# Performance work log

Hardware: AMD Instinct MI355X
Metric: run time of the kernel (lower is better)

Reference implementation:

```python
import jax, jax.numpy as jnp
import numpy as np

N = 50000   # nodes
E = 600000  # edges
D = 128     # in_neurons
H = 128     # hidden_neurons
O = 64      # output_neurons
G = 512     # graphs in batch
BN_EPS = 1e-5


def _linear_params(key, fan_in, fan_out):
    kw, kb = jax.random.split(key)
    s = 1.0 / np.sqrt(fan_in)
    W = jax.random.uniform(kw, (fan_out, fan_in), jnp.float32, -s, s)
    b = jax.random.uniform(kb, (fan_out,), jnp.float32, -s, s)
    return W, b


def setup_inputs() -> dict:
    key = jax.random.key(0)
    ks = jax.random.split(key, 12)
    inp = {}
    inp["x"] = jax.random.normal(ks[0], (N, D), jnp.float32)
    inp["edge_index"] = jax.random.randint(ks[1], (2, E), 0, N, jnp.int64)
    inp["batch"] = jnp.sort(jax.random.randint(ks[2], (N,), 0, G, jnp.int64))
    # GIN layer 1 (D->H->H), BN1
    inp["W11"], inp["b11"] = _linear_params(ks[3], D, H)
    inp["W12"], inp["b12"] = _linear_params(ks[4], H, H)
    inp["g1"], inp["be1"] = jnp.ones((H,), jnp.float32), jnp.zeros((H,), jnp.float32)
    # GIN layer 2
    inp["W21"], inp["b21"] = _linear_params(ks[5], H, H)
    inp["W22"], inp["b22"] = _linear_params(ks[6], H, H)
    inp["g2"], inp["be2"] = jnp.ones((H,), jnp.float32), jnp.zeros((H,), jnp.float32)
    # GIN layer 3
    inp["W31"], inp["b31"] = _linear_params(ks[7], H, H)
    inp["W32"], inp["b32"] = _linear_params(ks[8], H, H)
    inp["g3"], inp["be3"] = jnp.ones((H,), jnp.float32), jnp.zeros((H,), jnp.float32)
    # final projection (3H -> O)
    inp["linW"], inp["linb"] = _linear_params(ks[9], 3 * H, O)
    return inp


def reference(x, edge_index, batch,
              W11, b11, W12, b12, g1, be1,
              W21, b21, W22, b22, g2, be2,
              W31, b31, W32, b32, g3, be3,
              linW, linb):
    src, dst = edge_index[0], edge_index[1]

    def gin_conv(h, Wa, ba, Wb, bb):
        # GIN (eps=0): mlp((1+eps)*h + sum_{j in N(i)} h_j)
        agg = jax.ops.segment_sum(h[src], dst, num_segments=N)
        z = h + agg
        z = jax.nn.relu(z @ Wa.T + ba)
        return z @ Wb.T + bb

    def batch_norm(h, g, b):
        # training-mode BatchNorm1d: per-feature batch stats (biased var)
        mu = jnp.mean(h, axis=0)
        var = jnp.var(h, axis=0)
        return g * (h - mu) * jax.lax.rsqrt(var + BN_EPS) + b

    h1 = jax.nn.relu(batch_norm(gin_conv(x, W11, b11, W12, b12), g1, be1))
    h2 = jax.nn.relu(batch_norm(gin_conv(h1, W21, b21, W22, b22), g2, be2))
    h3 = jax.nn.relu(batch_norm(gin_conv(h2, W31, b31, W32, b32), g3, be3))

    counts = jax.ops.segment_sum(jnp.ones((N,), jnp.float32), batch, num_segments=G)
    counts = jnp.maximum(counts, 1.0)[:, None]  # [G, 1]

    def mean_pool(h):
        return jax.ops.segment_sum(h, batch, num_segments=G) / counts

    h_final = jnp.concatenate([mean_pool(h1), mean_pool(h2), mean_pool(h3)], axis=1)  # [G, 3H]
    out = h_final @ linW.T + linb  # [G, O]
    # F.normalize(dim=1): divide by L2 norm clamped to eps=1e-12
    nrm = jnp.maximum(jnp.linalg.norm(out, axis=1, keepdims=True), 1e-12)
    return out / nrm
```

## Files before the change

### kernel.cpp

```cpp
#include <hip/hip_runtime.h>

#define NN 50000
#define NE 600000
#define HD 128
#define NG 512
#define OD 64
#define BN_EPS 1e-5f

#define SCAN_BLK 1024
#define NSB ((NN + SCAN_BLK - 1) / SCAN_BLK)
#define ECAP 1536
#define NBANK 8

typedef __attribute__((ext_vector_type(8))) short bf16x8;
typedef __attribute__((ext_vector_type(4))) float f32x4;

__device__ __forceinline__ unsigned short f2bf(float f) {
    unsigned u = __builtin_bit_cast(unsigned, f);
    unsigned r = u + 0x7FFFu + ((u >> 16) & 1u);
    return (unsigned short)(r >> 16);
}

__device__ __forceinline__ float bflo(unsigned u) { return __builtin_bit_cast(float, u << 16); }
__device__ __forceinline__ float bfhi(unsigned u) { return __builtin_bit_cast(float, u & 0xffff0000u); }

__device__ __forceinline__ unsigned packbf2(float x, float y) {
    return (unsigned)f2bf(x) | ((unsigned)f2bf(y) << 16);
}


__global__ void cvt_kernel(const float* __restrict__ src, unsigned short* __restrict__ dst, int n8) {
    int i = blockIdx.x * blockDim.x + threadIdx.x;
    if (i >= n8) return;
    float4 a = ((const float4*)src)[2 * i];
    float4 b = ((const float4*)src)[2 * i + 1];
    uint4 o;
    o.x = packbf2(a.x, a.y);
    o.y = packbf2(a.z, a.w);
    o.z = packbf2(b.x, b.y);
    o.w = packbf2(b.z, b.w);
    ((uint4*)dst)[i] = o;
}

__global__ void cvt6_kernel(const float* __restrict__ s0, const float* __restrict__ s1,
                            const float* __restrict__ s2, const float* __restrict__ s3,
                            const float* __restrict__ s4, const float* __restrict__ s5,
                            unsigned short* __restrict__ dst) {
    int i = blockIdx.x * blockDim.x + threadIdx.x;
    const int wsel = i >> 11;
    const int o8 = i & 2047;
    const float* sp = (wsel == 0) ? s0 : (wsel == 1) ? s1 : (wsel == 2) ? s2
                    : (wsel == 3) ? s3 : (wsel == 4) ? s4 : s5;
    float4 a = ((const float4*)sp)[2 * o8];
    float4 b = ((const float4*)sp)[2 * o8 + 1];
    uint4 o;
    o.x = packbf2(a.x, a.y);
    o.y = packbf2(a.z, a.w);
    o.z = packbf2(b.x, b.y);
    o.w = packbf2(b.z, b.w);
    ((uint4*)(dst + (size_t)wsel * HD * HD))[o8] = o;
}


__global__ void hist_kernel(const int* __restrict__ dst, int* __restrict__ deg, int E) {
    int i = blockIdx.x * blockDim.x + threadIdx.x;
    if (i < E) atomicAdd(&deg[dst[i]], 1);
}

__global__ void local_scan_kernel(const int* __restrict__ deg, int* __restrict__ lexcl,
                                  int* __restrict__ bsum, int n) {
    __shared__ int part[SCAN_BLK];
    const int tid = threadIdx.x;
    const int i = blockIdx.x * SCAN_BLK + tid;
    int v = (i < n) ? deg[i] : 0;
    part[tid] = v;
    __syncthreads();
    int incl = v;
    for (int off = 1; off < SCAN_BLK; off <<= 1) {
        int t = (tid >= off) ? part[tid - off] : 0;
        __syncthreads();
        incl += t;
        part[tid] = incl;
        __syncthreads();
    }
    if (i < n) lexcl[i] = incl - v;
    if (tid == SCAN_BLK - 1) bsum[blockIdx.x] = incl;
}

__global__ void scan_bsum_kernel(const int* __restrict__ bsum, int* __restrict__ boff,
                                 int* __restrict__ offsets, int nb, int n) {
    const int tid = threadIdx.x;
    int orig = (tid < nb) ? bsum[tid] : 0;
    int v = orig;
    for (int off = 1; off < 64; off <<= 1) {
        int t = __shfl_up(v, off);
        if (tid >= off) v += t;
    }
    if (tid < nb) boff[tid] = v - orig;
    if (tid == 63) offsets[n] = v;
}

__global__ void finalize_gstart_kernel(const int* __restrict__ lexcl, const int* __restrict__ boff,
                                       int* __restrict__ offsets, int* __restrict__ cursor,
                                       const int* __restrict__ batch, int* __restrict__ gstart,
                                       int n, int G) {
    int i = blockIdx.x * blockDim.x + threadIdx.x;
    if (i >= n) return;
    int o = lexcl[i] + boff[i >> 10];
    offsets[i] = o;
    cursor[i] = o;
    int b = batch[i];
    int bp = (i == 0) ? -1 : batch[i - 1];
    for (int g = bp + 1; g <= b; ++g) gstart[g] = i;
    if (i == n - 1) {
        for (int g = b + 1; g <= G; ++g) gstart[g] = n;
    }
}

__global__ void fill_kernel(const int* __restrict__ src, const int* __restrict__ dst,
                            int* __restrict__ cursor, int* __restrict__ srcs, int E) {
    int i = blockIdx.x * blockDim.x + threadIdx.x;
    if (i < E) {
        int pos = atomicAdd(&cursor[dst[i]], 1);
        srcs[pos] = src[i];
    }
}


__global__ __launch_bounds__(512) void fused_gin(const unsigned* __restrict__ hp,
                                                 const int* __restrict__ offsets,
                                                 const int* __restrict__ srcs,
                                                 const unsigned short* __restrict__ WaBf,
                                                 const float* __restrict__ ba,
                                                 const unsigned short* __restrict__ WbBf,
                                                 const float* __restrict__ bb,
                                                 unsigned short* __restrict__ Cb,
                                                 float* __restrict__ statsOut,
                                                 int nrows) {
    __shared__ short SB[64 * 136];
    __shared__ int elds[ECAP];
    __shared__ float sred[2][128][2];

    const int t = threadIdx.x;
    const int lane = t & 63;
    const int w = t >> 6;
    const int g16 = lane >> 4;
    const int c16 = lane & 15;
    const int row0 = blockIdx.x * 64;

    const int rend = (row0 + 64 < nrows) ? row0 + 64 : nrows;
    const int ebase = offsets[row0];
    const int cnt = offsets[rend] - ebase;
    const bool fast = (cnt <= ECAP);

    if (fast) {
        for (int k = t; k < cnt; k += 512) elds[k] = srcs[ebase + k];
    }
    __syncthreads();

    for (int i = 0; i < 8; ++i) {
        const int r = w * 8 + i;
        const int grow = row0 + r;
        float a0 = 0.f, a1 = 0.f, a2 = 0.f, a3 = 0.f;
        float a4 = 0.f, a5 = 0.f, a6 = 0.f, a7 = 0.f;

        auto acc8 = [&](uint4 v) {
            a0 += bflo(v.x); a1 += bfhi(v.x);
            a2 += bflo(v.y); a3 += bfhi(v.y);
            a4 += bflo(v.z); a5 += bfhi(v.z);
            a6 += bflo(v.w); a7 += bfhi(v.w);
        };
        auto ld4 = [&](int idx) -> uint4 {
            return ((const uint4*)(hp + (size_t)idx * 64))[c16];
        };

        if (grow < nrows) {
            const int jb = offsets[grow];
            const int items = offsets[grow + 1] - jb + 1;
            if (fast) {
                const int j0 = jb - ebase;
                uint4 v0 = {0, 0, 0, 0}, v1 = {0, 0, 0, 0}, v2 = {0, 0, 0, 0}, v3 = {0, 0, 0, 0};
                {
                    const int it = g16;
                    if (it < items) v0 = ld4(it == 0 ? grow : elds[j0 + it - 1]);
                }
                {
                    const int it = 4 + g16;
                    if (it < items) v1 = ld4(elds[j0 + it - 1]);
                }
                {
                    const int it = 8 + g16;
                    if (it < items) v2 = ld4(elds[j0 + it - 1]);
                }
                {
                    const int it = 12 + g16;
                    if (it < items) v3 = ld4(elds[j0 + it - 1]);
                }
                acc8(v0); acc8(v1); acc8(v2); acc8(v3);
                for (int base = 16; base < items; base += 4) {
                    const int it = base + g16;
                    uint4 v = {0, 0, 0, 0};
                    if (it < items) v = ld4(elds[j0 + it - 1]);
                    acc8(v);
                }
            } else {
                for (int base = 0; base < items; base += 4) {
                    const int it = base + g16;
                    uint4 v = {0, 0, 0, 0};
                    if (it < items) v = ld4(it == 0 ? grow : srcs[jb + it - 1]);
                    acc8(v);
                }
            }
        }
        a0 += __shfl_xor(a0, 16); a1 += __shfl_xor(a1, 16);
        a2 += __shfl_xor(a2, 16); a3 += __shfl_xor(a3, 16);
        a4 += __shfl_xor(a4, 16); a5 += __shfl_xor(a5, 16);
        a6 += __shfl_xor(a6, 16); a7 += __shfl_xor(a7, 16);
        a0 += __shfl_xor(a0, 32); a1 += __shfl_xor(a1, 32);
        a2 += __shfl_xor(a2, 32); a3 += __shfl_xor(a3, 32);
        a4 += __shfl_xor(a4, 32); a5 += __shfl_xor(a5, 32);
        a6 += __shfl_xor(a6, 32); a7 += __shfl_xor(a7, 32);
        if (g16 == 0) {
            uint4 o;
            o.x = packbf2(a0, a1);
            o.y = packbf2(a2, a3);
            o.z = packbf2(a4, a5);
            o.w = packbf2(a6, a7);
            *(uint4*)&SB[r * 136 + c16 * 8] = o;
        }
    }
    __syncthreads();

    const int wr = w >> 2;
    const int wc = w & 3;
    const int l15 = lane & 15;
    const int l4 = lane >> 4;

    f32x4 acc[2][2];
#pragma unroll
    for (int m = 0; m < 2; ++m)
#pragma unroll
        for (int n = 0; n < 2; ++n) acc[m][n] = (f32x4){0.f, 0.f, 0.f, 0.f};

#pragma unroll
    for (int kk = 0; kk < 4; ++kk) {
        bf16x8 af[2], bfr[2];
#pragma unroll
        for (int m = 0; m < 2; ++m)
            af[m] = *(const bf16x8*)&SB[(wr * 32 + m * 16 + l15) * 136 + kk * 32 + l4 * 8];
#pragma unroll
        for (int n = 0; n < 2; ++n)
            bfr[n] = *(const bf16x8*)(WaBf + (size_t)(wc * 32 + n * 16 + l15) * HD + kk * 32 + l4 * 8);
#pragma unroll
        for (int m = 0; m < 2; ++m)
#pragma unroll
            for (int n = 0; n < 2; ++n)
                acc[m][n] = __builtin_amdgcn_mfma_f32_16x16x32_bf16(af[m], bfr[n], acc[m][n], 0, 0, 0);
    }
    __syncthreads();

#pragma unroll
    for (int n = 0; n < 2; ++n) {
        const int col = wc * 32 + n * 16 + l15;
        const float bav = ba[col];
#pragma unroll
        for (int m = 0; m < 2; ++m) {
#pragma unroll
            for (int j = 0; j < 4; ++j) {
                const int row = wr * 32 + m * 16 + l4 * 4 + j;
                SB[row * 136 + col] = (short)f2bf(fmaxf(acc[m][n][j] + bav, 0.f));
            }
        }
    }
    __syncthreads();

#pragma unroll
    for (int m = 0; m < 2; ++m)
#pragma unroll
        for (int n = 0; n < 2; ++n) acc[m][n] = (f32x4){0.f, 0.f, 0.f, 0.f};

#pragma unroll
    for (int kk = 0; kk < 4; ++kk) {
        bf16x8 af[2], bfr[2];
#pragma unroll
        for (int m = 0; m < 2; ++m)
            af[m] = *(const bf16x8*)&SB[(wr * 32 + m * 16 + l15) * 136 + kk * 32 + l4 * 8];
#pragma unroll
        for (int n = 0; n < 2; ++n)
            bfr[n] = *(const bf16x8*)(WbBf + (size_t)(wc * 32 + n * 16 + l15) * HD + kk * 32 + l4 * 8);
#pragma unroll
        for (int m = 0; m < 2; ++m)
#pragma unroll
            for (int n = 0; n < 2; ++n)
                acc[m][n] = __builtin_amdgcn_mfma_f32_16x16x32_bf16(af[m], bfr[n], acc[m][n], 0, 0, 0);
    }

    float st00 = 0.f, st01 = 0.f, st10 = 0.f, st11 = 0.f;
#pragma unroll
    for (int n = 0; n < 2; ++n) {
        const int col = wc * 32 + n * 16 + l15;
        const float bbv = bb[col];
#pragma unroll
        for (int m = 0; m < 2; ++m) {
#pragma unroll
            for (int j = 0; j < 4; ++j) {
                const int row = row0 + wr * 32 + m * 16 + l4 * 4 + j;
                if (row < nrows) {
                    float v = acc[m][n][j] + bbv;
                    Cb[(size_t)row * HD + col] = f2bf(v);
                    if (n == 0) { st00 += v; st01 = fmaf(v, v, st01); }
                    else        { st10 += v; st11 = fmaf(v, v, st11); }
                }
            }
        }
    }
#pragma unroll
    for (int d = 16; d < 64; d <<= 1) {
        st00 += __shfl_xor(st00, d);
        st01 += __shfl_xor(st01, d);
        st10 += __shfl_xor(st10, d);
        st11 += __shfl_xor(st11, d);
    }
    if (l4 == 0) {
        const int c0 = wc * 32 + l15, c1 = c0 + 16;
        sred[wr][c0][0] = st00; sred[wr][c0][1] = st01;
        sred[wr][c1][0] = st10; sred[wr][c1][1] = st11;
    }
    __syncthreads();
    if (t < 128) {
        float* so = statsOut + (blockIdx.x & (NBANK - 1)) * 256;
        atomicAdd(&so[t], sred[0][t][0] + sred[1][t][0]);
        atomicAdd(&so[128 + t], sred[0][t][1] + sred[1][t][1]);
    }
}


template <bool WR>
__global__ void pool_bn(const unsigned* __restrict__ hp, const int* __restrict__ gstart,
                        const float* __restrict__ stats, const float* __restrict__ gam,
                        const float* __restrict__ bet, float* __restrict__ pooled, int layerOff,
                        unsigned* __restrict__ hn) {
    __shared__ float sstat[256];
    __shared__ float wred[8][16][8];
    __shared__ float fin[128];

    const int g = blockIdx.x;
    const int tx = threadIdx.x;
    const int ch = tx & 15;
    const int q = tx >> 4;
    const int w = tx >> 6;
    const int lane = tx & 63;

    for (int k = tx; k < 256; k += 512) {
        float s = 0.f;
#pragma unroll
        for (int b = 0; b < NBANK; ++b) s += stats[b * 256 + k];
        sstat[k] = s;
    }
    __syncthreads();

    const float invn = 1.0f / (float)NN;
    float sc[8], sh[8];
#pragma unroll
    for (int k = 0; k < 8; ++k) {
        const int c = ch * 8 + k;
        float mu = sstat[c] * invn;
        float va = sstat[128 + c] * invn - mu * mu;
        sc[k] = gam[c] * rsqrtf(va + BN_EPS);
        sh[k] = bet[c] - mu * sc[k];
    }

    const int s0 = gstart[g], s1 = gstart[g + 1];
    float a[8];
#pragma unroll
    for (int k = 0; k < 8; ++k) a[k] = 0.f;

    for (int i = s0 + q; i < s1; i += 32) {
        uint4 u = ((const uint4*)(hp + (size_t)i * 64))[ch];
        float v0 = fmaxf(fmaf(bflo(u.x), sc[0], sh[0]), 0.f);
        float v1 = fmaxf(fmaf(bfhi(u.x), sc[1], sh[1]), 0.f);
        float v2 = fmaxf(fmaf(bflo(u.y), sc[2], sh[2]), 0.f);
        float v3 = fmaxf(fmaf(bfhi(u.y), sc[3], sh[3]), 0.f);
        float v4 = fmaxf(fmaf(bflo(u.z), sc[4], sh[4]), 0.f);
        float v5 = fmaxf(fmaf(bfhi(u.z), sc[5], sh[5]), 0.f);
        float v6 = fmaxf(fmaf(bflo(u.w), sc[6], sh[6]), 0.f);
        float v7 = fmaxf(fmaf(bfhi(u.w), sc[7], sh[7]), 0.f);
        if (WR) {
            uint4 o;
            o.x = packbf2(v0, v1);
            o.y = packbf2(v2, v3);
            o.z = packbf2(v4, v5);
            o.w = packbf2(v6, v7);
            ((uint4*)(hn + (size_t)i * 64))[ch] = o;
        }
        a[0] += v0; a[1] += v1; a[2] += v2; a[3] += v3;
        a[4] += v4; a[5] += v5; a[6] += v6; a[7] += v7;
    }

#pragma unroll
    for (int k = 0; k < 8; ++k) {
        a[k] += __shfl_xor(a[k], 16);
        a[k] += __shfl_xor(a[k], 32);
    }
    if ((lane >> 4) == 0) {
#pragma unroll
        for (int k = 0; k < 8; ++k) wred[w][ch][k] = a[k];
    }
    __syncthreads();

    const int cnt = s1 - s0;
    const float fc = (cnt > 0) ? (float)cnt : 1.0f;
    if (tx < 128) {
        float r = 0.f;
#pragma unroll
        for (int ww = 0; ww < 8; ++ww) r += wred[ww][tx >> 3][tx & 7];
        fin[tx] = r / fc;
    }
    __syncthreads();
    if (tx < 32) {
        float4 v = *(const float4*)&fin[tx * 4];
        *(float4*)&pooled[(size_t)g * (3 * HD) + layerOff + tx * 4] = v;
    }
}


__global__ void final_kernel(const float* __restrict__ pooled, const float* __restrict__ linW,
                             const float* __restrict__ linb, float* __restrict__ out) {
    __shared__ float p[3 * HD];
    const int g = blockIdx.x;
    const int o = threadIdx.x;
    for (int k = o; k < 3 * HD; k += 64) p[k] = pooled[(size_t)g * (3 * HD) + k];
    __syncthreads();
    float acc = linb[o];
    const float* wrow = linW + (size_t)o * (3 * HD);
#pragma unroll 4
    for (int k = 0; k < 3 * HD; k += 4) {
        float4 wv = *(const float4*)(wrow + k);
        float4 pv = *(const float4*)(&p[k]);
        acc = fmaf(wv.x, pv.x, acc);
        acc = fmaf(wv.y, pv.y, acc);
        acc = fmaf(wv.z, pv.z, acc);
        acc = fmaf(wv.w, pv.w, acc);
    }
    float sq = acc * acc;
#pragma unroll
    for (int off = 32; off > 0; off >>= 1) sq += __shfl_xor(sq, off);
    float nrm = sqrtf(sq);
    nrm = fmaxf(nrm, 1e-12f);
    out[(size_t)g * OD + o] = acc / nrm;
}


extern "C" void kernel_launch(void* const* d_in, const int* in_sizes, int n_in,
                              void* d_out, int out_size, void* d_ws, size_t ws_size,
                              hipStream_t stream) {
    const float* x    = (const float*)d_in[0];
    const int* ei     = (const int*)d_in[1];
    const int* batch  = (const int*)d_in[2];
    const float* W11  = (const float*)d_in[3];
    const float* b11  = (const float*)d_in[4];
    const float* W12  = (const float*)d_in[5];
    const float* b12  = (const float*)d_in[6];
    const float* g1   = (const float*)d_in[7];
    const float* be1  = (const float*)d_in[8];
    const float* W21  = (const float*)d_in[9];
    const float* b21  = (const float*)d_in[10];
    const float* W22  = (const float*)d_in[11];
    const float* b22  = (const float*)d_in[12];
    const float* g2   = (const float*)d_in[13];
    const float* be2  = (const float*)d_in[14];
    const float* W31  = (const float*)d_in[15];
    const float* b31  = (const float*)d_in[16];
    const float* W32  = (const float*)d_in[17];
    const float* b32  = (const float*)d_in[18];
    const float* g3   = (const float*)d_in[19];
    const float* be3  = (const float*)d_in[20];
    const float* linW = (const float*)d_in[21];
    const float* linb = (const float*)d_in[22];

    const int* src = ei;
    const int* dst = ei + NE;

    char* ws = (char*)d_ws;
    size_t off = 0;
    auto alloc = [&](size_t bytes) -> void* {
        void* p = ws + off;
        off += (bytes + 255) & ~(size_t)255;
        return p;
    };
    int* deg      = (int*)alloc((size_t)NN * 4);
    int* offsets  = (int*)alloc((size_t)(NN + 1) * 4);
    int* cursor   = (int*)alloc((size_t)NN * 4);
    int* srcs     = (int*)alloc((size_t)NE * 4);
    int* gstart   = (int*)alloc((size_t)(NG + 1) * 4);
    int* lexcl    = (int*)alloc((size_t)NN * 4);
    int* bsum     = (int*)alloc((size_t)NSB * 4);
    int* boff     = (int*)alloc((size_t)NSB * 4);
    float* stats  = (float*)alloc((size_t)3 * NBANK * 256 * 4);
    float* pooled = (float*)alloc((size_t)NG * 3 * HD * 4);
    unsigned short* xbf  = (unsigned short*)alloc((size_t)NN * HD * 2);
    unsigned short* cbf1 = (unsigned short*)alloc((size_t)NN * HD * 2);
    unsigned short* cbf2 = (unsigned short*)alloc((size_t)NN * HD * 2);
    unsigned short* hbf1 = (unsigned short*)alloc((size_t)NN * HD * 2);
    unsigned short* hbf2 = (unsigned short*)alloc((size_t)NN * HD * 2);
    unsigned short* wbf  = (unsigned short*)alloc((size_t)6 * HD * HD * 2);
    (void)ws_size; (void)n_in; (void)in_sizes; (void)out_size;

    cvt_kernel<<<(NN * HD / 8 + 255) / 256, 256, 0, stream>>>(x, xbf, NN * HD / 8);
    cvt6_kernel<<<48, 256, 0, stream>>>(W11, W12, W21, W22, W31, W32, wbf);

    hipMemsetAsync(deg, 0, (size_t)NN * 4, stream);
    hist_kernel<<<(NE + 255) / 256, 256, 0, stream>>>(dst, deg, NE);
    local_scan_kernel<<<NSB, SCAN_BLK, 0, stream>>>(deg, lexcl, bsum, NN);
    scan_bsum_kernel<<<1, 64, 0, stream>>>(bsum, boff, offsets, NSB, NN);
    finalize_gstart_kernel<<<(NN + 255) / 256, 256, 0, stream>>>(lexcl, boff, offsets, cursor,
                                                                 batch, gstart, NN, NG);
    fill_kernel<<<(NE + 255) / 256, 256, 0, stream>>>(src, dst, cursor, srcs, NE);

    hipMemsetAsync(stats, 0, (size_t)3 * NBANK * 256 * 4, stream);

    const int ginGrid = (NN + 63) / 64;

    const unsigned* xu  = (const unsigned*)xbf;
    const unsigned* c1u = (const unsigned*)cbf1;
    const unsigned* c2u = (const unsigned*)cbf2;
    const unsigned* h1u = (const unsigned*)hbf1;
    const unsigned* h2u = (const unsigned*)hbf2;

    float* st1 = stats;
    float* st2 = stats + NBANK * 256;
    float* st3 = stats + 2 * NBANK * 256;

    fused_gin<<<ginGrid, 512, 0, stream>>>(xu, offsets, srcs,
                                           wbf + 0 * HD * HD, b11, wbf + 1 * HD * HD, b12,
                                           cbf1, st1, NN);
    pool_bn<true><<<NG, 512, 0, stream>>>(c1u, gstart, st1, g1, be1, pooled, 0, (unsigned*)hbf1);

    fused_gin<<<ginGrid, 512, 0, stream>>>(h1u, offsets, srcs,
                                           wbf + 2 * HD * HD, b21, wbf + 3 * HD * HD, b22,
                                           cbf2, st2, NN);
    pool_bn<true><<<NG, 512, 0, stream>>>(c2u, gstart, st2, g2, be2, pooled, HD, (unsigned*)hbf2);

    fused_gin<<<ginGrid, 512, 0, stream>>>(h2u, offsets, srcs,
                                           wbf + 4 * HD * HD, b31, wbf + 5 * HD * HD, b32,
                                           cbf1, st3, NN);
    pool_bn<false><<<NG, 512, 0, stream>>>(c1u, gstart, st3, g3, be3, pooled, 2 * HD, nullptr);

    final_kernel<<<NG, OD, 0, stream>>>(pooled, linW, linb, (float*)d_out);
}
```

Baseline: 236.6 us.

## Split fused GIN kernel into separate gather and MLP kernels

Replaces the fused aggregation-plus-MLP kernel with two kernels. A grid-stride gather kernel uses one wave per node and writes the aggregated bf16 features to a global buffer. An MLP kernel then reads those features directly from global memory into the MFMA GEMMs. The aim is to decouple the irregular, latency-bound gather from the compute phase so each can run at its own occupancy. The cost is an extra round trip of the full N×128 bf16 intermediate through global memory, one extra launch per layer, and loss of the LDS-staged edge list.

Result: slower. 270.9 us (+14.5%).

```diff
diff --git a/kernel.cpp b/kernel.cpp
--- a/kernel.cpp
+++ b/kernel.cpp
@@ -9,7 +9,6 @@
 
 #define SCAN_BLK 1024
 #define NSB ((NN + SCAN_BLK - 1) / SCAN_BLK)
-#define ECAP 1536
 #define NBANK 8
 
 typedef __attribute__((ext_vector_type(8))) short bf16x8;
@@ -127,91 +126,60 @@
 }
 
 
-__global__ __launch_bounds__(512) void fused_gin(const unsigned* __restrict__ hp,
-                                                 const int* __restrict__ offsets,
-                                                 const int* __restrict__ srcs,
-                                                 const unsigned short* __restrict__ WaBf,
-                                                 const float* __restrict__ ba,
-                                                 const unsigned short* __restrict__ WbBf,
-                                                 const float* __restrict__ bb,
-                                                 unsigned short* __restrict__ Cb,
-                                                 float* __restrict__ statsOut,
-                                                 int nrows) {
-    __shared__ short SB[64 * 136];
-    __shared__ int elds[ECAP];
-    __shared__ float sred[2][128][2];
-
+__global__ __launch_bounds__(1024) void gather_kernel(const unsigned* __restrict__ hp,
+                                                      const int* __restrict__ offsets,
+                                                      const int* __restrict__ srcs,
+                                                      unsigned* __restrict__ z, int nrows) {
     const int t = threadIdx.x;
     const int lane = t & 63;
     const int w = t >> 6;
     const int g16 = lane >> 4;
     const int c16 = lane & 15;
-    const int row0 = blockIdx.x * 64;
-
-    const int rend = (row0 + 64 < nrows) ? row0 + 64 : nrows;
-    const int ebase = offsets[row0];
-    const int cnt = offsets[rend] - ebase;
-    const bool fast = (cnt <= ECAP);
-
-    if (fast) {
-        for (int k = t; k < cnt; k += 512) elds[k] = srcs[ebase + k];
-    }
-    __syncthreads();
-
-    for (int i = 0; i < 8; ++i) {
-        const int r = w * 8 + i;
-        const int grow = row0 + r;
+    const int waveId = blockIdx.x * 16 + w;
+    const int nWaves = gridDim.x * 16;
+
+    auto ld4 = [&](int idx) -> uint4 {
+        return ((const uint4*)(hp + (size_t)idx * 64))[c16];
+    };
+
+    for (int node = waveId; node < nrows; node += nWaves) {
+        const int jb = offsets[node];
+        const int items = offsets[node + 1] - jb + 1;
+
         float a0 = 0.f, a1 = 0.f, a2 = 0.f, a3 = 0.f;
         float a4 = 0.f, a5 = 0.f, a6 = 0.f, a7 = 0.f;
-
         auto acc8 = [&](uint4 v) {
             a0 += bflo(v.x); a1 += bfhi(v.x);
             a2 += bflo(v.y); a3 += bfhi(v.y);
             a4 += bflo(v.z); a5 += bfhi(v.z);
             a6 += bflo(v.w); a7 += bfhi(v.w);
         };
-        auto ld4 = [&](int idx) -> uint4 {
-            return ((const uint4*)(hp + (size_t)idx * 64))[c16];
-        };
-
-        if (grow < nrows) {
-            const int jb = offsets[grow];
-            const int items = offsets[grow + 1] - jb + 1;
-            if (fast) {
-                const int j0 = jb - ebase;
-                uint4 v0 = {0, 0, 0, 0}, v1 = {0, 0, 0, 0}, v2 = {0, 0, 0, 0}, v3 = {0, 0, 0, 0};
-                {
-                    const int it = g16;
-                    if (it < items) v0 = ld4(it == 0 ? grow : elds[j0 + it - 1]);
-                }
-                {
-                    const int it = 4 + g16;
-                    if (it < items) v1 = ld4(elds[j0 + it - 1]);
-                }
-                {
-                    const int it = 8 + g16;
-                    if (it < items) v2 = ld4(elds[j0 + it - 1]);
-                }
-                {
-                    const int it = 12 + g16;
-                    if (it < items) v3 = ld4(elds[j0 + it - 1]);
-                }
-                acc8(v0); acc8(v1); acc8(v2); acc8(v3);
-                for (int base = 16; base < items; base += 4) {
-                    const int it = base + g16;
-                    uint4 v = {0, 0, 0, 0};
-                    if (it < items) v = ld4(elds[j0 + it - 1]);
-                    acc8(v);
-                }
-            } else {
-                for (int base = 0; base < items; base += 4) {
-                    const int it = base + g16;
-                    uint4 v = {0, 0, 0, 0};
-                    if (it < items) v = ld4(it == 0 ? grow : srcs[jb + it - 1]);
-                    acc8(v);
-                }
-            }
-        }
+
+        uint4 v0 = {0, 0, 0, 0}, v1 = {0, 0, 0, 0}, v2 = {0, 0, 0, 0}, v3 = {0, 0, 0, 0};
+        {
+            const int it = g16;
+            if (it < items) v0 = ld4(it == 0 ? node : srcs[jb + it - 1]);
+        }
+        {
+            const int it = 4 + g16;
+            if (it < items) v1 = ld4(srcs[jb + it - 1]);
+        }
+        {
+            const int it = 8 + g16;
+            if (it < items) v2 = ld4(srcs[jb + it - 1]);
+        }
+        {
+            const int it = 12 + g16;
+            if (it < items) v3 = ld4(srcs[jb + it - 1]);
+        }
+        acc8(v0); acc8(v1); acc8(v2); acc8(v3);
+        for (int base = 16; base < items; base += 4) {
+            const int it = base + g16;
+            uint4 v = {0, 0, 0, 0};
+            if (it < items) v = ld4(srcs[jb + it - 1]);
+            acc8(v);
+        }
+
         a0 += __shfl_xor(a0, 16); a1 += __shfl_xor(a1, 16);
         a2 += __shfl_xor(a2, 16); a3 += __shfl_xor(a3, 16);
         a4 += __shfl_xor(a4, 16); a5 += __shfl_xor(a5, 16);
@@ -226,16 +194,34 @@
             o.y = packbf2(a2, a3);
             o.z = packbf2(a4, a5);
             o.w = packbf2(a6, a7);
-            *(uint4*)&SB[r * 136 + c16 * 8] = o;
-        }
-    }
-    __syncthreads();
-
+            ((uint4*)(z + (size_t)node * 64))[c16] = o;
+        }
+    }
+}
+
+
+__global__ __launch_bounds__(512) void mlp_kernel(const unsigned short* __restrict__ Zb,
+                                                  const unsigned short* __restrict__ WaBf,
+                                                  const float* __restrict__ ba,
+                                                  const unsigned short* __restrict__ WbBf,
+                                                  const float* __restrict__ bb,
+                                                  unsigned short* __restrict__ Cb,
+                                                  float* __restrict__ statsOut,
+                                                  int nrows) {
+    __shared__ short A2[64 * 136];
+    __shared__ float sred[2][128][2];
+
+    const int t = threadIdx.x;
+    const int lane = t & 63;
+    const int w = t >> 6;
+    const int row0 = blockIdx.x * 64;
     const int wr = w >> 2;
     const int wc = w & 3;
     const int l15 = lane & 15;
     const int l4 = lane >> 4;
 
+    const bf16x8 zero8 = {0, 0, 0, 0, 0, 0, 0, 0};
+
     f32x4 acc[2][2];
 #pragma unroll
     for (int m = 0; m < 2; ++m)
@@ -246,8 +232,12 @@
     for (int kk = 0; kk < 4; ++kk) {
         bf16x8 af[2], bfr[2];
 #pragma unroll
-        for (int m = 0; m < 2; ++m)
-            af[m] = *(const bf16x8*)&SB[(wr * 32 + m * 16 + l15) * 136 + kk * 32 + l4 * 8];
+        for (int m = 0; m < 2; ++m) {
+            const int row = row0 + wr * 32 + m * 16 + l15;
+            af[m] = (row < nrows)
+                  ? *(const bf16x8*)(Zb + (size_t)row * HD + kk * 32 + l4 * 8)
+                  : zero8;
+        }
 #pragma unroll
         for (int n = 0; n < 2; ++n)
             bfr[n] = *(const bf16x8*)(WaBf + (size_t)(wc * 32 + n * 16 + l15) * HD + kk * 32 + l4 * 8);
@@ -257,7 +247,6 @@
             for (int n = 0; n < 2; ++n)
                 acc[m][n] = __builtin_amdgcn_mfma_f32_16x16x32_bf16(af[m], bfr[n], acc[m][n], 0, 0, 0);
     }
-    __syncthreads();
 
 #pragma unroll
     for (int n = 0; n < 2; ++n) {
@@ -268,7 +257,7 @@
 #pragma unroll
             for (int j = 0; j < 4; ++j) {
                 const int row = wr * 32 + m * 16 + l4 * 4 + j;
-                SB[row * 136 + col] = (short)f2bf(fmaxf(acc[m][n][j] + bav, 0.f));
+                A2[row * 136 + col] = (short)f2bf(fmaxf(acc[m][n][j] + bav, 0.f));
             }
         }
     }
@@ -284,7 +273,7 @@
         bf16x8 af[2], bfr[2];
 #pragma unroll
         for (int m = 0; m < 2; ++m)
-            af[m] = *(const bf16x8*)&SB[(wr * 32 + m * 16 + l15) * 136 + kk * 32 + l4 * 8];
+            af[m] = *(const bf16x8*)&A2[(wr * 32 + m * 16 + l15) * 136 + kk * 32 + l4 * 8];
 #pragma unroll
         for (int n = 0; n < 2; ++n)
             bfr[n] = *(const bf16x8*)(WbBf + (size_t)(wc * 32 + n * 16 + l15) * HD + kk * 32 + l4 * 8);
@@ -499,6 +488,7 @@
     float* stats  = (float*)alloc((size_t)3 * NBANK * 256 * 4);
     float* pooled = (float*)alloc((size_t)NG * 3 * HD * 4);
     unsigned short* xbf  = (unsigned short*)alloc((size_t)NN * HD * 2);
+    unsigned short* zbf  = (unsigned short*)alloc((size_t)NN * HD * 2);
     unsigned short* cbf1 = (unsigned short*)alloc((size_t)NN * HD * 2);
     unsigned short* cbf2 = (unsigned short*)alloc((size_t)NN * HD * 2);
     unsigned short* hbf1 = (unsigned short*)alloc((size_t)NN * HD * 2);
@@ -519,9 +509,10 @@
 
     hipMemsetAsync(stats, 0, (size_t)3 * NBANK * 256 * 4, stream);
 
-    const int ginGrid = (NN + 63) / 64;
+    const int mlpGrid = (NN + 63) / 64;
 
     const unsigned* xu  = (const unsigned*)xbf;
+    unsigned* zu        = (unsigned*)zbf;
     const unsigned* c1u = (const unsigned*)cbf1;
     const unsigned* c2u = (const unsigned*)cbf2;
     const unsigned* h1u = (const unsigned*)hbf1;
@@ -531,19 +522,19 @@
     float* st2 = stats + NBANK * 256;
     float* st3 = stats + 2 * NBANK * 256;
 
-    fused_gin<<<ginGrid, 512, 0, stream>>>(xu, offsets, srcs,
-                                           wbf + 0 * HD * HD, b11, wbf + 1 * HD * HD, b12,
-                                           cbf1, st1, NN);
+    gather_kernel<<<512, 1024, 0, stream>>>(xu, offsets, srcs, zu, NN);
+    mlp_kernel<<<mlpGrid, 512, 0, stream>>>(zbf, wbf + 0 * HD * HD, b11, wbf + 1 * HD * HD, b12,
+                                            cbf1, st1, NN);
     pool_bn<true><<<NG, 512, 0, stream>>>(c1u, gstart, st1, g1, be1, pooled, 0, (unsigned*)hbf1);
 
-    fused_gin<<<ginGrid, 512, 0, stream>>>(h1u, offsets, srcs,
-                                           wbf + 2 * HD * HD, b21, wbf + 3 * HD * HD, b22,
-                                           cbf2, st2, NN);
+    gather_kernel<<<512, 1024, 0, stream>>>(h1u, offsets, srcs, zu, NN);
+    mlp_kernel<<<mlpGrid, 512, 0, stream>>>(zbf, wbf + 2 * HD * HD, b21, wbf + 3 * HD * HD, b22,
+                                            cbf2, st2, NN);
     pool_bn<true><<<NG, 512, 0, stream>>>(c2u, gstart, st2, g2, be2, pooled, HD, (unsigned*)hbf2);
 
-    fused_gin<<<ginGrid, 512, 0, stream>>>(h2u, offsets, srcs,
-                                           wbf + 4 * HD * HD, b31, wbf + 5 * HD * HD, b32,
-                                           cbf1, st3, NN);
+    gather_kernel<<<512, 1024, 0, stream>>>(h2u, offsets, srcs, zu, NN);
+    mlp_kernel<<<mlpGrid, 512, 0, stream>>>(zbf, wbf + 4 * HD * HD, b31, wbf + 5 * HD * HD, b32,
+                                            cbf1, st3, NN);
     pool_bn<false><<<NG, 512, 0, stream>>>(c1u, gstart, st3, g3, be3, pooled, 2 * HD, nullptr);
 
     final_kernel<<<NG, OD, 0, stream>>>(pooled, linW, linb, (float*)d_out);
```
